# Performance work log

Hardware: AMD Instinct MI355X
Metric: run time of the kernel (lower is better)

## Reference

```python
import jax, jax.numpy as jnp
import numpy as np

ANCHORS = np.array([[10.0, 13.0], [16.0, 30.0], [33.0, 23.0]], dtype=np.float32)
IMG_W, IMG_H = 416.0, 416.0
NUM_CLASSES = 80
NUM_ANCHORS = 3
IGNORE_THR = 0.5
LAMBDA_IOU, LAMBDA_CONF, LAMBDA_CLS = 0.5, 1.0, 1.0
EPS = 1e-7


def _bce(p, t):
    p = jnp.clip(p, EPS, 1.0 - EPS)
    return -(t * jnp.log(p) + (1.0 - t) * jnp.log(1.0 - p))


def _xywh_iou(x1, y1, w1, h1, x2, y2, w2, h2):
    iw = jnp.clip(jnp.minimum(x1 + w1 * 0.5, x2 + w2 * 0.5) - jnp.maximum(x1 - w1 * 0.5, x2 - w2 * 0.5), 0.0)
    ih = jnp.clip(jnp.minimum(y1 + h1 * 0.5, y2 + h2 * 0.5) - jnp.maximum(y1 - h1 * 0.5, y2 - h2 * 0.5), 0.0)
    inter = iw * ih
    return inter / (w1 * h1 + w2 * h2 - inter + 1e-16)


def _decode(targets, anchors, in_w, in_h):
    # Vectorized version of the per-target python loop. Scatter with
    # out-of-bounds indices (default 'drop' mode) skips invalid/empty targets.
    B, T = targets.shape[0], targets.shape[1]
    A = anchors.shape[0]
    valid = jnp.sum(targets, axis=-1) != 0  # [B,T]
    gx = targets[..., 1] * in_w
    gy = targets[..., 2] * in_h
    gw = targets[..., 3] * in_w
    gh = targets[..., 4] * in_h
    gi = gx.astype(jnp.int32)
    gj = gy.astype(jnp.int32)
    cls = targets[..., 0].astype(jnp.int32)
    aw, ah = anchors[:, 0], anchors[:, 1]
    # anchor-vs-gt IoU at origin (center format): [B,T,A]
    inter = jnp.minimum(gw[..., None], aw) * jnp.minimum(gh[..., None], ah)
    anch_iou = inter / (gw[..., None] * gh[..., None] + aw * ah - inter + 1e-16)
    best_n = jnp.argmax(anch_iou, axis=-1)  # [B,T]
    gi_s = jnp.where(valid, gi, in_w)  # invalid -> OOB -> dropped
    gj_s = jnp.where(valid, gj, in_h)
    bb = jnp.broadcast_to(jnp.arange(B)[:, None], (B, T))
    shape = (B, A, in_h, in_w)
    zeros = jnp.zeros(shape, jnp.float32)
    # noobj: zero out every anchor with IoU > thr at the gt cell
    bb3 = jnp.broadcast_to(jnp.arange(B)[:, None, None], (B, T, A))
    aa3 = jnp.broadcast_to(jnp.arange(A)[None, None, :], (B, T, A))
    gj3 = jnp.broadcast_to(gj_s[..., None], (B, T, A))
    gi3 = jnp.broadcast_to(gi_s[..., None], (B, T, A))
    noobj = jnp.ones(shape, jnp.float32).at[bb3, aa3, gj3, gi3].min(
        jnp.where(anch_iou > IGNORE_THR, 0.0, 1.0))
    scat = lambda v: zeros.at[bb, best_n, gj_s, gi_s].set(v)
    mask = zeros.at[bb, best_n, gj_s, gi_s].max(jnp.ones_like(gx))
    tx = scat(gx - gi.astype(jnp.float32))
    ty = scat(gy - gj.astype(jnp.float32))
    tw = scat(jnp.log(gw / aw[best_n] + 1e-16))
    th = scat(jnp.log(gh / ah[best_n] + 1e-16))
    kx, ky, kw, kh = scat(gx), scat(gy), scat(gw), scat(gh)
    tconf = mask
    tcls = jnp.zeros(shape + (NUM_CLASSES,), jnp.float32).at[bb, best_n, gj_s, gi_s, cls].set(1.0)
    return mask, noobj, tx, ty, tw, th, kx, ky, kw, kh, tconf, tcls


def reference(input, targets):
    bs, _, in_h, in_w = input.shape
    stride_h = IMG_H / in_h
    stride_w = IMG_W / in_w
    scaled = jnp.asarray(ANCHORS) / jnp.array([stride_w, stride_h], jnp.float32)  # [A,2]
    pred = input.reshape(bs, NUM_ANCHORS, 5 + NUM_CLASSES, in_h, in_w).transpose(0, 1, 3, 4, 2)
    x = jax.nn.sigmoid(pred[..., 0])
    y = jax.nn.sigmoid(pred[..., 1])
    w = pred[..., 2]
    h = pred[..., 3]
    conf = jax.nn.sigmoid(pred[..., 4])
    pred_cls = jax.nn.sigmoid(pred[..., 5:])
    dec = _decode(targets, scaled, in_w, in_h)
    # targets in torch are requires_grad=False buffers -> constants
    mask, noobj, tx, ty, tw, th, kx, ky, kw, kh, tconf, tcls = [jax.lax.stop_gradient(t) for t in dec]
    grid_x = jnp.arange(in_w, dtype=jnp.float32)[None, None, None, :]
    grid_y = jnp.arange(in_h, dtype=jnp.float32)[None, None, :, None]
    anchor_w = scaled[:, 0][None, :, None, None]
    anchor_h = scaled[:, 1][None, :, None, None]
    # torch uses x.data / w.data -> detached box decode, no grad through IoU loss
    hx = jax.lax.stop_gradient(x) + grid_x
    hy = jax.lax.stop_gradient(y) + grid_y
    hw = jnp.exp(jax.lax.stop_gradient(w)) * anchor_w
    hh = jnp.exp(jax.lax.stop_gradient(h)) * anchor_h
    iou = _xywh_iou(hx, hy, hw, hh, kx, ky, kw, kh)
    loss_iou = jnp.sum((1.0 - iou) * mask)
    loss_conf = jnp.mean(_bce(conf * mask, mask)) + 0.5 * jnp.mean(_bce(conf * noobj, jnp.zeros_like(noobj)))
    n_pos = jnp.maximum(jnp.sum(mask), 1.0)
    # BCELoss mean over the mask==1 positions only (n_pos * C elements)
    loss_cls = jnp.sum(_bce(pred_cls, tcls) * mask[..., None]) / (n_pos * NUM_CLASSES)
    loss = loss_iou * LAMBDA_IOU + loss_conf * LAMBDA_CONF + loss_cls * LAMBDA_CLS
    return loss, loss_iou, loss_conf, loss_cls


def setup_inputs() -> dict:
    key = jax.random.key(0)
    k1, k2, k3, k4 = jax.random.split(key, 4)
    B, T = 32, 50
    inp = jax.random.normal(k1, (B, 255, 52, 52), dtype=jnp.float32) * 0.5
    cls = jnp.floor(jax.random.uniform(k2, (B, T, 1)) * NUM_CLASSES)
    xy = jax.random.uniform(k3, (B, T, 2), minval=0.02, maxval=0.98)
    wh = jax.random.uniform(k4, (B, T, 2), minval=0.05, maxval=0.30)
    targets = jnp.concatenate([cls, xy, wh], axis=-1).astype(jnp.float32)
    return {"input": inp, "targets": targets}
```

## Files before the change

### kernel.cpp

```cpp
#include <hip/hip_runtime.h>
#include <stdint.h>

#define BATCH 32
#define NA 3
#define GH 52
#define GW 52
#define NT 50
#define NCLS 80
#define HW_ (GH * GW)
#define NCELL (BATCH * NA * HW_)
#define NBLKX ((HW_ + 255) / 256)
#define NBA (BATCH * NA)
#define NPART (NBA * NBLKX)
#define FEPS 1e-7f

__device__ __forceinline__ float sigmf(float x) { return 1.0f / (1.0f + expf(-x)); }

__device__ __forceinline__ float bcef(float p, float t) {
    p = fminf(fmaxf(p, FEPS), 1.0f - FEPS);
    return -(t * logf(p) + (1.0f - t) * logf(1.0f - p));
}

__global__ __launch_bounds__(256) void k_main(const float* __restrict__ in,
                                              const float* __restrict__ tg,
                                              float* __restrict__ part) {
    __shared__ int    sinfo[NT];
    __shared__ float4 sbox[NT];
    __shared__ float  red[4][5];

    const int tid = threadIdx.x;
    const int ba  = blockIdx.y;
    const int b   = ba / NA;
    const int a   = ba - b * NA;

    if (tid < NT) {
        const float* p = tg + (b * NT + tid) * 5;
        float f0 = p[0], f1 = p[1], f2 = p[2], f3 = p[3], f4 = p[4];
        int info = 0;
        float gx = f1 * GW, gy = f2 * GH, gw = f3 * GW, gh = f4 * GH;
        int gi = (int)gx, gj = (int)gy, cls = (int)f0;
        bool valid = (f0 + f1 + f2 + f3 + f4) != 0.0f &&
                     gi >= 0 && gi < GW && gj >= 0 && gj < GH &&
                     cls >= 0 && cls < NCLS;
        if (valid) {
            const float aw0 = 1.25f, aw1 = 2.0f, aw2 = 4.125f;
            const float ah0 = 1.625f, ah1 = 3.75f, ah2 = 2.875f;
            float ga = gw * gh;
            float i0 = fminf(gw, aw0) * fminf(gh, ah0); float u0 = i0 / (ga + aw0 * ah0 - i0 + 1e-16f);
            float i1 = fminf(gw, aw1) * fminf(gh, ah1); float u1 = i1 / (ga + aw1 * ah1 - i1 + 1e-16f);
            float i2 = fminf(gw, aw2) * fminf(gh, ah2); float u2 = i2 / (ga + aw2 * ah2 - i2 + 1e-16f);
            int bn = 0; float best = u0;
            if (u1 > best) { best = u1; bn = 1; }
            if (u2 > best) { best = u2; bn = 2; }
            int thr = (u0 > 0.5f ? 1 : 0) | (u1 > 0.5f ? 2 : 0) | (u2 > 0.5f ? 4 : 0);
            info = gi | (gj << 6) | (bn << 12) | (thr << 14) | (1 << 17) | (cls << 18);
            sbox[tid] = make_float4(gx, gy, gw, gh);
        }
        sinfo[tid] = info;
    }
    __syncthreads();

    const int ji = blockIdx.x * 256 + tid;
    float iou_t = 0.f, t1 = 0.f, t2 = 0.f, cls_t = 0.f, m = 0.f;
    if (ji < HW_) {
        const int i = ji % GW, j = ji / GW;
        float no = 1.0f, KX = 0.f, KY = 0.f, KW = 0.f, KH = 0.f;
        uint32_t cw0 = 0, cw1 = 0, cw2 = 0;
        bool pos = false;
        for (int t = 0; t < NT; ++t) {
            int inf = sinfo[t];
            if (!(inf & (1 << 17))) continue;
            if ((inf & 63) != i || ((inf >> 6) & 63) != j) continue;
            if (((inf >> 14) >> a) & 1) no = 0.0f;
            if (((inf >> 12) & 3) == a) {
                pos = true;
                float4 bx = sbox[t];
                KX = bx.x; KY = bx.y; KW = bx.z; KH = bx.w;
                int cls = (inf >> 18) & 127;
                if (cls < 32)      cw0 |= 1u << cls;
                else if (cls < 64) cw1 |= 1u << (cls - 32);
                else               cw2 |= 1u << (cls - 64);
            }
        }
        m = pos ? 1.0f : 0.0f;
        const float* base = in + ((size_t)ba * 85) * HW_ + ji;
        float conf = sigmf(base[4 * HW_]);
        t1 = bcef(conf * m, m);
        t2 = bcef(conf * no, 0.0f);
        if (pos) {
            float hx = sigmf(base[0]) + (float)i;
            float hy = sigmf(base[HW_]) + (float)j;
            float aw = (a == 0) ? 1.25f  : (a == 1) ? 2.0f  : 4.125f;
            float ah = (a == 0) ? 1.625f : (a == 1) ? 3.75f : 2.875f;
            float hw = expf(base[2 * HW_]) * aw;
            float hh = expf(base[3 * HW_]) * ah;
            float iw = fmaxf(fminf(hx + hw * 0.5f, KX + KW * 0.5f) -
                             fmaxf(hx - hw * 0.5f, KX - KW * 0.5f), 0.f);
            float ih = fmaxf(fminf(hy + hh * 0.5f, KY + KH * 0.5f) -
                             fmaxf(hy - hh * 0.5f, KY - KH * 0.5f), 0.f);
            float inter = iw * ih;
            float iou = inter / (hw * hh + KW * KH - inter + 1e-16f);
            iou_t = 1.0f - iou;
            #pragma unroll 4
            for (int c = 0; c < NCLS; ++c) {
                float pc = sigmf(base[(5 + c) * HW_]);
                uint32_t bit = (c < 32) ? ((cw0 >> c) & 1u)
                             : (c < 64) ? ((cw1 >> (c - 32)) & 1u)
                                        : ((cw2 >> (c - 64)) & 1u);
                cls_t += bcef(pc, (float)bit);
            }
        }
    }

    #pragma unroll
    for (int off = 32; off > 0; off >>= 1) {
        iou_t += __shfl_down(iou_t, off, 64);
        t1    += __shfl_down(t1,    off, 64);
        t2    += __shfl_down(t2,    off, 64);
        cls_t += __shfl_down(cls_t, off, 64);
        m     += __shfl_down(m,     off, 64);
    }
    const int wv = tid >> 6;
    if ((tid & 63) == 0) {
        red[wv][0] = iou_t; red[wv][1] = t1; red[wv][2] = t2;
        red[wv][3] = cls_t; red[wv][4] = m;
    }
    __syncthreads();
    if (tid == 0) {
        float s0 = 0.f, s1 = 0.f, s2 = 0.f, s3 = 0.f, s4 = 0.f;
        #pragma unroll
        for (int w = 0; w < 4; ++w) {
            s0 += red[w][0]; s1 += red[w][1]; s2 += red[w][2];
            s3 += red[w][3]; s4 += red[w][4];
        }
        float* pp = part + ((size_t)ba * NBLKX + blockIdx.x) * 5;
        pp[0] = s0; pp[1] = s1; pp[2] = s2; pp[3] = s3; pp[4] = s4;
    }
}

__global__ __launch_bounds__(256) void k_final(const float* __restrict__ part,
                                               float* __restrict__ out) {
    __shared__ float red[4][5];
    int tid = threadIdx.x;
    float s0 = 0.f, s1 = 0.f, s2 = 0.f, s3 = 0.f, s4 = 0.f;
    for (int p = tid; p < NPART; p += 256) {
        const float* pp = part + (size_t)p * 5;
        s0 += pp[0]; s1 += pp[1]; s2 += pp[2]; s3 += pp[3]; s4 += pp[4];
    }
    #pragma unroll
    for (int off = 32; off > 0; off >>= 1) {
        s0 += __shfl_down(s0, off, 64);
        s1 += __shfl_down(s1, off, 64);
        s2 += __shfl_down(s2, off, 64);
        s3 += __shfl_down(s3, off, 64);
        s4 += __shfl_down(s4, off, 64);
    }
    int wv = tid >> 6;
    if ((tid & 63) == 0) {
        red[wv][0] = s0; red[wv][1] = s1; red[wv][2] = s2;
        red[wv][3] = s3; red[wv][4] = s4;
    }
    __syncthreads();
    if (tid == 0) {
        float a0 = 0.f, a1 = 0.f, a2 = 0.f, a3 = 0.f, a4 = 0.f;
        #pragma unroll
        for (int w = 0; w < 4; ++w) {
            a0 += red[w][0]; a1 += red[w][1]; a2 += red[w][2];
            a3 += red[w][3]; a4 += red[w][4];
        }
        const float N = (float)NCELL;
        float loss_iou  = a0;
        float loss_conf = a1 / N + 0.5f * (a2 / N);
        float npos      = fmaxf(a4, 1.0f);
        float loss_cls  = a3 / (npos * (float)NCLS);
        float loss = 0.5f * loss_iou + loss_conf + loss_cls;
        out[0] = loss; out[1] = loss_iou; out[2] = loss_conf; out[3] = loss_cls;
    }
}

extern "C" void kernel_launch(void* const* d_in, const int* in_sizes, int n_in,
                              void* d_out, int out_size, void* d_ws, size_t ws_size,
                              hipStream_t stream) {
    const float* input   = (const float*)d_in[0];
    const float* targets = (const float*)d_in[1];
    float* out  = (float*)d_out;
    float* part = (float*)d_ws;

    dim3 grid(NBLKX, NBA);
    k_main <<<grid, 256, 0, stream>>>(input, targets, part);
    k_final<<<1, 256, 0, stream>>>(part, out);
}
```

Before: 156.8 us.

## Split loss into dense conf-channel pass and sparse per-target positive/ignore pass

Restructures the kernel so the dense part only reads the confidence channel with float4 loads and computes the noobj BCE via softplus algebra. Positive cells and ignore-cells are enumerated sparsely from the target list, deduplicated per cell, and handled by wavefronts that read the 85 channels of each positive cell. This avoids scanning all 50 targets for every grid cell and avoids touching class channels for the many empty cells. The trade-off is more complex deduplication logic and BCE clamping approximated through softplus plus epsilon corrections, which changes numerics slightly.

```diff
diff --git a/kernel.cpp b/kernel.cpp
--- a/kernel.cpp
+++ b/kernel.cpp
@@ -9,132 +9,204 @@
 #define NCLS 80
 #define HW_ (GH * GW)
 #define NCELL (BATCH * NA * HW_)
-#define NBLKX ((HW_ + 255) / 256)
 #define NBA (BATCH * NA)
-#define NPART (NBA * NBLKX)
-#define FEPS 1e-7f
-
-__device__ __forceinline__ float sigmf(float x) { return 1.0f / (1.0f + expf(-x)); }
-
-__device__ __forceinline__ float bcef(float p, float t) {
-    p = fminf(fmaxf(p, FEPS), 1.0f - FEPS);
-    return -(t * logf(p) + (1.0f - t) * logf(1.0f - p));
+#define CQUAD (HW_ / 4)
+#define NQUAD (NBA * CQUAD)
+#define PHASEA_BLOCKS 256
+#define NCHUNK 4
+#define CHUNK 13
+#define PHASEB_BLOCKS (BATCH * NCHUNK)
+#define NPART (PHASEA_BLOCKS + PHASEB_BLOCKS)
+#define CEPS 1.0000000494e-07f
+
+__device__ __forceinline__ float sp(float z) {
+    return fmaxf(z, 0.f) + log1pf(expf(-fabsf(z)));
+}
+__device__ __forceinline__ float sigmf(float x) { return 1.f / (1.f + expf(-x)); }
+
+__device__ __forceinline__ float wred(float v) {
+    #pragma unroll
+    for (int o = 32; o > 0; o >>= 1) v += __shfl_down(v, o, 64);
+    return v;
 }
 
 __global__ __launch_bounds__(256) void k_main(const float* __restrict__ in,
                                               const float* __restrict__ tg,
                                               float* __restrict__ part) {
-    __shared__ int    sinfo[NT];
-    __shared__ float4 sbox[NT];
-    __shared__ float  red[4][5];
-
-    const int tid = threadIdx.x;
-    const int ba  = blockIdx.y;
-    const int b   = ba / NA;
-    const int a   = ba - b * NA;
-
-    if (tid < NT) {
-        const float* p = tg + (b * NT + tid) * 5;
-        float f0 = p[0], f1 = p[1], f2 = p[2], f3 = p[3], f4 = p[4];
-        int info = 0;
-        float gx = f1 * GW, gy = f2 * GH, gw = f3 * GW, gh = f4 * GH;
-        int gi = (int)gx, gj = (int)gy, cls = (int)f0;
-        bool valid = (f0 + f1 + f2 + f3 + f4) != 0.0f &&
-                     gi >= 0 && gi < GW && gj >= 0 && gj < GH &&
-                     cls >= 0 && cls < NCLS;
-        if (valid) {
-            const float aw0 = 1.25f, aw1 = 2.0f, aw2 = 4.125f;
-            const float ah0 = 1.625f, ah1 = 3.75f, ah2 = 2.875f;
-            float ga = gw * gh;
-            float i0 = fminf(gw, aw0) * fminf(gh, ah0); float u0 = i0 / (ga + aw0 * ah0 - i0 + 1e-16f);
-            float i1 = fminf(gw, aw1) * fminf(gh, ah1); float u1 = i1 / (ga + aw1 * ah1 - i1 + 1e-16f);
-            float i2 = fminf(gw, aw2) * fminf(gh, ah2); float u2 = i2 / (ga + aw2 * ah2 - i2 + 1e-16f);
-            int bn = 0; float best = u0;
-            if (u1 > best) { best = u1; bn = 1; }
-            if (u2 > best) { best = u2; bn = 2; }
-            int thr = (u0 > 0.5f ? 1 : 0) | (u1 > 0.5f ? 2 : 0) | (u2 > 0.5f ? 4 : 0);
-            info = gi | (gj << 6) | (bn << 12) | (thr << 14) | (1 << 17) | (cls << 18);
-            sbox[tid] = make_float4(gx, gy, gw, gh);
-        }
-        sinfo[tid] = info;
-    }
-    __syncthreads();
-
-    const int ji = blockIdx.x * 256 + tid;
-    float iou_t = 0.f, t1 = 0.f, t2 = 0.f, cls_t = 0.f, m = 0.f;
-    if (ji < HW_) {
-        const int i = ji % GW, j = ji / GW;
-        float no = 1.0f, KX = 0.f, KY = 0.f, KW = 0.f, KH = 0.f;
-        uint32_t cw0 = 0, cw1 = 0, cw2 = 0;
-        bool pos = false;
-        for (int t = 0; t < NT; ++t) {
-            int inf = sinfo[t];
-            if (!(inf & (1 << 17))) continue;
-            if ((inf & 63) != i || ((inf >> 6) & 63) != j) continue;
-            if (((inf >> 14) >> a) & 1) no = 0.0f;
-            if (((inf >> 12) & 3) == a) {
-                pos = true;
-                float4 bx = sbox[t];
-                KX = bx.x; KY = bx.y; KW = bx.z; KH = bx.w;
-                int cls = (inf >> 18) & 127;
-                if (cls < 32)      cw0 |= 1u << cls;
-                else if (cls < 64) cw1 |= 1u << (cls - 32);
-                else               cw2 |= 1u << (cls - 64);
-            }
-        }
-        m = pos ? 1.0f : 0.0f;
-        const float* base = in + ((size_t)ba * 85) * HW_ + ji;
-        float conf = sigmf(base[4 * HW_]);
-        t1 = bcef(conf * m, m);
-        t2 = bcef(conf * no, 0.0f);
-        if (pos) {
-            float hx = sigmf(base[0]) + (float)i;
-            float hy = sigmf(base[HW_]) + (float)j;
-            float aw = (a == 0) ? 1.25f  : (a == 1) ? 2.0f  : 4.125f;
-            float ah = (a == 0) ? 1.625f : (a == 1) ? 3.75f : 2.875f;
-            float hw = expf(base[2 * HW_]) * aw;
-            float hh = expf(base[3 * HW_]) * ah;
-            float iw = fmaxf(fminf(hx + hw * 0.5f, KX + KW * 0.5f) -
-                             fmaxf(hx - hw * 0.5f, KX - KW * 0.5f), 0.f);
-            float ih = fmaxf(fminf(hy + hh * 0.5f, KY + KH * 0.5f) -
-                             fmaxf(hy - hh * 0.5f, KY - KH * 0.5f), 0.f);
+    __shared__ float red[4][5];
+    const int bid = blockIdx.x, tid = threadIdx.x;
+    float s0 = 0.f, s1 = 0.f, s2 = 0.f, s3 = 0.f, s4 = 0.f;
+
+    if (bid < PHASEA_BLOCKS) {
+        int idx = bid * 256 + tid;
+        if (idx < NQUAD) {
+            int ba = idx / CQUAD, q = idx - ba * CQUAD;
+            const float4* cp = reinterpret_cast<const float4*>(
+                in + ((size_t)(ba * 85 + 4)) * HW_);
+            float4 v = cp[q];
+            s2 = sp(v.x) + sp(v.y) + sp(v.z) + sp(v.w);
+        }
+    } else {
+        __shared__ int    sinfo[NT];
+        __shared__ float4 sbox[NT];
+        __shared__ int    plist_info[CHUNK];
+        __shared__ float4 plist_box[CHUNK];
+        __shared__ uint32_t plist_c[CHUNK][3];
+        __shared__ int    nolist[3 * CHUNK];
+        __shared__ int    cnt[2];
+
+        const int pb = bid - PHASEA_BLOCKS;
+        const int b  = pb / NCHUNK;
+        const int ch = pb - b * NCHUNK;
+        if (tid == 0) { cnt[0] = 0; cnt[1] = 0; }
+
+        if (tid < NT) {
+            const float* p = tg + (b * NT + tid) * 5;
+            float f0 = p[0], f1 = p[1], f2 = p[2], f3 = p[3], f4 = p[4];
+            int info = 0;
+            float gx = f1 * GW, gy = f2 * GH, gw = f3 * GW, gh = f4 * GH;
+            int gi = (int)gx, gj = (int)gy, cls = (int)f0;
+            bool valid = (f0 + f1 + f2 + f3 + f4) != 0.0f &&
+                         gi >= 0 && gi < GW && gj >= 0 && gj < GH;
+            if (valid) {
+                const float aw0 = 1.25f, aw1 = 2.0f, aw2 = 4.125f;
+                const float ah0 = 1.625f, ah1 = 3.75f, ah2 = 2.875f;
+                float ga = gw * gh;
+                float i0 = fminf(gw, aw0) * fminf(gh, ah0); float u0 = i0 / (ga + aw0 * ah0 - i0 + 1e-16f);
+                float i1 = fminf(gw, aw1) * fminf(gh, ah1); float u1 = i1 / (ga + aw1 * ah1 - i1 + 1e-16f);
+                float i2 = fminf(gw, aw2) * fminf(gh, ah2); float u2 = i2 / (ga + aw2 * ah2 - i2 + 1e-16f);
+                int bn = 0; float best = u0;
+                if (u1 > best) { best = u1; bn = 1; }
+                if (u2 > best) { best = u2; bn = 2; }
+                int thr = (u0 > 0.5f ? 1 : 0) | (u1 > 0.5f ? 2 : 0) | (u2 > 0.5f ? 4 : 0);
+                int clp = cls < 0 ? 0 : (cls > 127 ? 127 : cls);
+                info = gi | (gj << 6) | (bn << 12) | (thr << 14) | (1 << 17) | (clp << 18)
+                       | ((cls >= 0 && cls < NCLS) ? (1 << 25) : 0);
+                sbox[tid] = make_float4(gx, gy, gw, gh);
+            }
+            sinfo[tid] = info;
+        }
+        __syncthreads();
+
+        if (tid < CHUNK) {
+            int t = ch * CHUNK + tid;
+            if (t < NT) {
+                int inf = sinfo[t];
+                if (inf & (1 << 17)) {
+                    int key = inf & 0x3FFF;
+                    bool owner = true;
+                    for (int t2 = t + 1; t2 < NT; ++t2) {
+                        int i2 = sinfo[t2];
+                        if ((i2 & (1 << 17)) && ((i2 & 0x3FFF) == key)) { owner = false; break; }
+                    }
+                    if (owner) {
+                        uint32_t c0 = 0, c1 = 0, c2 = 0;
+                        for (int t2 = 0; t2 < NT; ++t2) {
+                            int i2 = sinfo[t2];
+                            if ((i2 & (1 << 17)) && ((i2 & 0x3FFF) == key) && (i2 & (1 << 25))) {
+                                int cl = (i2 >> 18) & 127;
+                                if (cl < 32)      c0 |= 1u << cl;
+                                else if (cl < 64) c1 |= 1u << (cl - 32);
+                                else if (cl < NCLS) c2 |= 1u << (cl - 64);
+                            }
+                        }
+                        int slot = atomicAdd(&cnt[0], 1);
+                        plist_info[slot] = inf; plist_box[slot] = sbox[t];
+                        plist_c[slot][0] = c0; plist_c[slot][1] = c1; plist_c[slot][2] = c2;
+                    }
+                }
+            }
+        }
+        if (tid < 3 * CHUNK) {
+            int t = ch * CHUNK + tid / 3, a = tid % 3;
+            if (t < NT) {
+                int inf = sinfo[t];
+                if ((inf & (1 << 17)) && ((inf >> (14 + a)) & 1)) {
+                    bool owner = true;
+                    for (int t2 = 0; t2 < t; ++t2) {
+                        int i2 = sinfo[t2];
+                        if ((i2 & (1 << 17)) && ((i2 & 0xFFF) == (inf & 0xFFF)) &&
+                            ((i2 >> (14 + a)) & 1)) { owner = false; break; }
+                    }
+                    if (owner) {
+                        int slot = atomicAdd(&cnt[1], 1);
+                        nolist[slot] = (inf & 0xFFF) | (a << 12);
+                    }
+                }
+            }
+        }
+        __syncthreads();
+
+        const int wv = tid >> 6, lane = tid & 63;
+        const int npos = cnt[0], nno = cnt[1];
+
+        for (int c = wv; c < npos; c += 4) {
+            int inf = plist_info[c];
+            int gi = inf & 63, gj = (inf >> 6) & 63, bn = (inf >> 12) & 3;
+            const float* base = in + ((size_t)((b * NA + bn) * 85)) * HW_ + (gj * GW + gi);
+            float v0 = base[lane * HW_];
+            float v1 = (lane < 21) ? base[(64 + lane) * HW_] : 0.f;
+            float z0 = __shfl(v0, 0, 64), z1 = __shfl(v0, 1, 64);
+            float z2 = __shfl(v0, 2, 64), z3 = __shfl(v0, 3, 64);
+            float z4 = __shfl(v0, 4, 64);
+            float aw = (bn == 0) ? 1.25f  : (bn == 1) ? 2.0f  : 4.125f;
+            float ah = (bn == 0) ? 1.625f : (bn == 1) ? 3.75f : 2.875f;
+            float hx = sigmf(z0) + (float)gi, hy = sigmf(z1) + (float)gj;
+            float hw = expf(z2) * aw,         hh = expf(z3) * ah;
+            float4 bx = plist_box[c];
+            float iw = fmaxf(fminf(hx + hw * .5f, bx.x + bx.z * .5f) -
+                             fmaxf(hx - hw * .5f, bx.x - bx.z * .5f), 0.f);
+            float ih = fmaxf(fminf(hy + hh * .5f, bx.y + bx.w * .5f) -
+                             fmaxf(hy - hh * .5f, bx.y - bx.w * .5f), 0.f);
             float inter = iw * ih;
-            float iou = inter / (hw * hh + KW * KH - inter + 1e-16f);
-            iou_t = 1.0f - iou;
-            #pragma unroll 4
-            for (int c = 0; c < NCLS; ++c) {
-                float pc = sigmf(base[(5 + c) * HW_]);
-                uint32_t bit = (c < 32) ? ((cw0 >> c) & 1u)
-                             : (c < 64) ? ((cw1 >> (c - 32)) & 1u)
-                                        : ((cw2 >> (c - 64)) & 1u);
-                cls_t += bcef(pc, (float)bit);
-            }
-        }
-    }
-
-    #pragma unroll
-    for (int off = 32; off > 0; off >>= 1) {
-        iou_t += __shfl_down(iou_t, off, 64);
-        t1    += __shfl_down(t1,    off, 64);
-        t2    += __shfl_down(t2,    off, 64);
-        cls_t += __shfl_down(cls_t, off, 64);
-        m     += __shfl_down(m,     off, 64);
-    }
-    const int wv = tid >> 6;
+            float iou = inter / (hw * hh + bx.z * bx.w - inter + 1e-16f);
+            uint32_t c0 = plist_c[c][0], c1 = plist_c[c][1], c2 = plist_c[c][2];
+            float contrib = 0.f;
+            if (lane >= 5) {
+                int cl = lane - 5;
+                uint32_t bit = (cl < 32) ? ((c0 >> cl) & 1u)
+                             : (cl < 64) ? ((c1 >> (cl - 32)) & 1u)
+                                         : ((c2 >> (cl - 64)) & 1u);
+                contrib += bit ? sp(-v0) : sp(v0);
+            }
+            if (lane < 21) {
+                int cl = 59 + lane;
+                uint32_t bit = (cl < 64) ? ((c1 >> (cl - 32)) & 1u)
+                                         : ((c2 >> (cl - 64)) & 1u);
+                contrib += bit ? sp(-v1) : sp(v1);
+            }
+            float tot = wred(contrib);
+            if (lane == 0) {
+                s3 += tot;
+                s0 += 1.0f - iou;
+                s1 += sp(-z4) - CEPS;
+                s4 += 1.0f;
+            }
+        }
+        for (int k = tid; k < nno; k += 256) {
+            int e = nolist[k];
+            int gi = e & 63, gj = (e >> 6) & 63, a = e >> 12;
+            float z = in[((size_t)((b * NA + a) * 85 + 4)) * HW_ + (gj * GW + gi)];
+            s2 += CEPS - sp(z);
+        }
+    }
+
+    s0 = wred(s0); s1 = wred(s1); s2 = wred(s2); s3 = wred(s3); s4 = wred(s4);
+    const int wv2 = tid >> 6;
     if ((tid & 63) == 0) {
-        red[wv][0] = iou_t; red[wv][1] = t1; red[wv][2] = t2;
-        red[wv][3] = cls_t; red[wv][4] = m;
+        red[wv2][0] = s0; red[wv2][1] = s1; red[wv2][2] = s2;
+        red[wv2][3] = s3; red[wv2][4] = s4;
     }
     __syncthreads();
     if (tid == 0) {
-        float s0 = 0.f, s1 = 0.f, s2 = 0.f, s3 = 0.f, s4 = 0.f;
+        float a0 = 0, a1 = 0, a2 = 0, a3 = 0, a4 = 0;
         #pragma unroll
         for (int w = 0; w < 4; ++w) {
-            s0 += red[w][0]; s1 += red[w][1]; s2 += red[w][2];
-            s3 += red[w][3]; s4 += red[w][4];
-        }
-        float* pp = part + ((size_t)ba * NBLKX + blockIdx.x) * 5;
-        pp[0] = s0; pp[1] = s1; pp[2] = s2; pp[3] = s3; pp[4] = s4;
+            a0 += red[w][0]; a1 += red[w][1]; a2 += red[w][2];
+            a3 += red[w][3]; a4 += red[w][4];
+        }
+        float* pp = part + (size_t)bid * 5;
+        pp[0] = a0; pp[1] = a1; pp[2] = a2; pp[3] = a3; pp[4] = a4;
     }
 }
 
@@ -142,19 +214,12 @@
                                                float* __restrict__ out) {
     __shared__ float red[4][5];
     int tid = threadIdx.x;
-    float s0 = 0.f, s1 = 0.f, s2 = 0.f, s3 = 0.f, s4 = 0.f;
+    float s0 = 0, s1 = 0, s2 = 0, s3 = 0, s4 = 0;
     for (int p = tid; p < NPART; p += 256) {
         const float* pp = part + (size_t)p * 5;
         s0 += pp[0]; s1 += pp[1]; s2 += pp[2]; s3 += pp[3]; s4 += pp[4];
     }
-    #pragma unroll
-    for (int off = 32; off > 0; off >>= 1) {
-        s0 += __shfl_down(s0, off, 64);
-        s1 += __shfl_down(s1, off, 64);
-        s2 += __shfl_down(s2, off, 64);
-        s3 += __shfl_down(s3, off, 64);
-        s4 += __shfl_down(s4, off, 64);
-    }
+    s0 = wred(s0); s1 = wred(s1); s2 = wred(s2); s3 = wred(s3); s4 = wred(s4);
     int wv = tid >> 6;
     if ((tid & 63) == 0) {
         red[wv][0] = s0; red[wv][1] = s1; red[wv][2] = s2;
@@ -162,7 +227,7 @@
     }
     __syncthreads();
     if (tid == 0) {
-        float a0 = 0.f, a1 = 0.f, a2 = 0.f, a3 = 0.f, a4 = 0.f;
+        float a0 = 0, a1 = 0, a2 = 0, a3 = 0, a4 = 0;
         #pragma unroll
         for (int w = 0; w < 4; ++w) {
             a0 += red[w][0]; a1 += red[w][1]; a2 += red[w][2];
@@ -170,7 +235,7 @@
         }
         const float N = (float)NCELL;
         float loss_iou  = a0;
-        float loss_conf = a1 / N + 0.5f * (a2 / N);
+        float loss_conf = ((float)NCELL * CEPS + a1) / N + 0.5f * (a2 / N);
         float npos      = fmaxf(a4, 1.0f);
         float loss_cls  = a3 / (npos * (float)NCLS);
         float loss = 0.5f * loss_iou + loss_conf + loss_cls;
@@ -186,7 +251,6 @@
     float* out  = (float*)d_out;
     float* part = (float*)d_ws;
 
-    dim3 grid(NBLKX, NBA);
-    k_main <<<grid, 256, 0, stream>>>(input, targets, part);
+    k_main <<<NPART, 256, 0, stream>>>(input, targets, part);
     k_final<<<1, 256, 0, stream>>>(part, out);
 }
```

Measured after the change: 133.0 us. 1.18x faster.
